# Performance work log

Hardware: AMD Instinct MI355X
Metric: run time of the kernel (lower is better)

Reference implementation:

```python
import jax, jax.numpy as jnp
import numpy as np

EUCLIDEAN_DIM = 6
B = 1024


def _build_tables(n):
    # CGA: basis vectors e1..en, e+, e-, diagonal metric (+1)*(n+1), (-1)
    d = n + 2
    nb = 1 << d
    metric = [1] * (n + 1) + [-1]
    # clifford orders blades by (grade, lexicographic) == (popcount, bitmask)
    masks = sorted(range(nb), key=lambda m: (bin(m).count('1'), m))
    pos = {m: i for i, m in enumerate(masks)}

    def sign_of(a, b):
        # canonical reordering sign + metric contractions for common vectors
        s = 1
        aa = a >> 1
        cnt = 0
        while aa:
            cnt += bin(aa & b).count('1')
            aa >>= 1
        if cnt & 1:
            s = -s
        common = a & b
        i = 0
        while common:
            if (common & 1) and metric[i] < 0:
                s = -s
            common >>= 1
            i += 1
        return s

    nnz = nb * nb  # every basis-blade product is one signed blade (nondegenerate metric)
    left = np.empty(nnz, np.int32)
    right = np.empty(nnz, np.int32)
    res = np.empty(nnz, np.int32)
    sgn = np.empty(nnz, np.int32)
    t = 0
    for i in range(nb):
        ma = masks[i]
        for j in range(nb):
            mb = masks[j]
            left[t] = i
            right[t] = j
            res[t] = pos[ma ^ mb]
            sgn[t] = sign_of(ma, mb)
            t += 1
    grades = np.array([bin(m).count('1') for m in masks])
    point_mask = np.where(grades == 1)[0].astype(np.int32)           # grade-1 blades
    pseudo = pos[nb - 1]
    motor_mask = np.where((grades % 2 == 0) & (np.arange(nb) != pseudo))[0].astype(np.int32)
    rev = ((-1) ** ((grades * (grades - 1)) // 2)).astype(np.int32)  # reverse signs
    motor_rev = rev[motor_mask]
    return left, right, res, sgn, point_mask, motor_mask, motor_rev


def setup_inputs() -> dict:
    key = jax.random.key(0)
    k1, k2 = jax.random.split(key)
    left, right, res, sgn, pmask, mmask, mrev = _build_tables(EUCLIDEAN_DIM)
    motor = jax.random.normal(k1, (B, mmask.shape[0]), jnp.float32)
    x = jax.random.normal(k2, (B, EUCLIDEAN_DIM), jnp.float32)
    return {
        'motor': motor,
        'x': x,
        'left_idx': jnp.asarray(left),
        'right_idx': jnp.asarray(right),
        'result_idx': jnp.asarray(res),
        'signs': jnp.asarray(sgn),
        'point_mask': jnp.asarray(pmask),
        'motor_mask': jnp.asarray(mmask),
        'motor_reverse_signs': jnp.asarray(mrev),
    }


def _gp(a, b, left_idx, right_idx, result_idx, signs_f, nb):
    # gather-multiply-scatter geometric product (same pattern as torch scatter_add)
    prod = signs_f * a[:, left_idx] * b[:, right_idx]  # (B, nnz)
    return jnp.zeros((a.shape[0], nb), a.dtype).at[:, result_idx].add(prod)


def reference(motor, x, left_idx, right_idx, result_idx, signs, point_mask, motor_mask, motor_reverse_signs):
    n = EUCLIDEAN_DIM
    nb = 1 << (n + 2)
    signs_f = signs.astype(jnp.float32)
    # UPGC encode: X = [x, -0.5 + 0.5|x|^2, 0.5 + 0.5|x|^2]
    h = 0.5 * jnp.sum(x * x, axis=-1, keepdims=True)
    point = jnp.concatenate([x, h - 0.5, h + 0.5], axis=-1)  # (B, n+2)
    Bsz = motor.shape[0]
    motor_full = jnp.zeros((Bsz, nb), jnp.float32).at[:, motor_mask].set(motor)
    point_full = jnp.zeros((Bsz, nb), jnp.float32).at[:, point_mask].set(point)
    motor_rev = motor * motor_reverse_signs.astype(jnp.float32)
    motor_rev_full = jnp.zeros((Bsz, nb), jnp.float32).at[:, motor_mask].set(motor_rev)
    # sandwich product M X M~ via two sparse geometric products
    mx = _gp(motor_full, point_full, left_idx, right_idx, result_idx, signs_f, nb)
    out_full = _gp(mx, motor_rev_full, left_idx, right_idx, result_idx, signs_f, nb)
    transformed = out_full[:, point_mask]  # (B, n+2)
    # UPGC decode: first n components
    return transformed[:, :n]
```

## Files before the change

### kernel.cpp

```cpp
#include <hip/hip_runtime.h>

#define NB   256
#define NM   127
#define NP   8
#define ND   6


constexpr int popc8(int x) { int c = 0; while (x) { c += x & 1; x >>= 1; } return c; }

constexpr int sign_of(int a, int b) {
    int s = 1;
    int aa = a >> 1, cnt = 0;
    while (aa) { cnt += popc8(aa & b); aa >>= 1; }
    if (cnt & 1) s = -s;
    int common = a & b, i = 0;
    while (common) {
        if ((common & 1) && i == 7) s = -s;
        common >>= 1; ++i;
    }
    return s;
}

struct Tables {
    alignas(16) int firstT[NB * 8];
    alignas(16) int secondT[128 * 8];
    alignas(16) int mpacked[128];
    alignas(16) int invm[NB];
};

constexpr Tables build_tables() {
    Tables T{};
    int masks[NB] = {}, pos[NB] = {};
    int t = 0;
    for (int pc = 0; pc <= 8; ++pc)
        for (int m = 0; m < NB; ++m)
            if (popc8(m) == pc) masks[t++] = m;
    for (int i = 0; i < NB; ++i) pos[masks[i]] = i;

    for (int i = 0; i < NB; ++i)
        for (int k = 0; k < NP; ++k) {
            int pp = 1 + k;
            int m  = pos[masks[i] ^ masks[pp]];
            int s  = sign_of(masks[m], masks[pp]);
            T.firstT[i * 8 + k] = (m << 1) | (s < 0 ? 1 : 0);
        }

    for (int i = 0; i < NB; ++i) T.invm[i] = -1;
    int j = 0;
    for (int i = 0; i < NB; ++i) {
        int g = popc8(masks[i]);
        if ((g % 2 == 0) && masks[i] != 255) {
            int rev = ((g * (g - 1) / 2) % 2) ? -1 : 1;
            T.mpacked[j] = (i << 1) | (rev < 0 ? 1 : 0);
            T.invm[i] = j;
            for (int r = 0; r < ND; ++r) {
                int rp = 1 + r;
                int ii = pos[masks[rp] ^ masks[i]];
                int s  = sign_of(masks[ii], masks[i]);
                T.secondT[j * 8 + r] = (ii << 1) | (s < 0 ? 1 : 0);
            }
            T.secondT[j * 8 + 6] = 0;
            T.secondT[j * 8 + 7] = 0;
            ++j;
        }
    }
    return T;
}

constexpr Tables hT = build_tables();
__device__ const Tables dT = hT;

__global__ __launch_bounds__(256) void cga_apply(
    const float* __restrict__ motor,
    const float* __restrict__ x,
    float*       __restrict__ out)
{
    __shared__ float m_full[NB];
    __shared__ float mx[NB];
    __shared__ float xs[ND];
    __shared__ float wpart[4][ND];

    const int t = threadIdx.x;
    const int b = blockIdx.x;

    const int4* ft = (const int4*)dT.firstT;
    int4 f0 = ft[2 * t];
    int4 f1 = ft[2 * t + 1];

    float mv = 0.0f;
    int   mp = 0;
    int4  s0 = {0,0,0,0}, s1 = {0,0,0,0};
    if (t < NM) {
        mv = motor[b * NM + t];
        mp = dT.mpacked[t];
        const int4* st = (const int4*)dT.secondT;
        s0 = st[2 * t];
        s1 = st[2 * t + 1];
    }
    if (t < ND) xs[t] = x[b * ND + t];

    const int im = dT.invm[t];
    m_full[t] = (im >= 0) ? motor[b * NM + im] : 0.0f;
    __syncthreads();

    float pv[NP];
    float h = 0.0f;
    #pragma unroll
    for (int k = 0; k < ND; ++k) { float v = xs[k]; pv[k] = v; h += v * v; }
    h *= 0.5f;
    pv[6] = h - 0.5f;
    pv[7] = h + 0.5f;

    int fe[8] = { f0.x, f0.y, f0.z, f0.w, f1.x, f1.y, f1.z, f1.w };
    float acc = 0.0f;
    #pragma unroll
    for (int k = 0; k < NP; ++k) {
        int   m = fe[k] >> 1;
        float v = m_full[m] * pv[k];
        acc += (fe[k] & 1) ? -v : v;
    }
    mx[t] = acc;
    __syncthreads();

    float o[ND] = {0,0,0,0,0,0};
    if (t < NM) {
        float mr = (mp & 1) ? -mv : mv;
        int se[ND] = { s0.x, s0.y, s0.z, s0.w, s1.x, s1.y };
        #pragma unroll
        for (int r = 0; r < ND; ++r) {
            int   i = se[r] >> 1;
            float v = mx[i] * mr;
            o[r] += (se[r] & 1) ? -v : v;
        }
    }

    #pragma unroll
    for (int r = 0; r < ND; ++r) {
        float v = o[r];
        #pragma unroll
        for (int d = 32; d >= 1; d >>= 1) v += __shfl_down(v, d, 64);
        o[r] = v;
    }
    const int lane = t & 63, w = t >> 6;
    if (lane == 0) {
        #pragma unroll
        for (int r = 0; r < ND; ++r) wpart[w][r] = o[r];
    }
    __syncthreads();

    if (t < ND)
        out[b * ND + t] = wpart[0][t] + wpart[1][t] + wpart[2][t] + wpart[3][t];
}

extern "C" void kernel_launch(void* const* d_in, const int* in_sizes, int n_in,
                              void* d_out, int out_size, void* d_ws, size_t ws_size,
                              hipStream_t stream) {
    const float* motor = (const float*)d_in[0];
    const float* x     = (const float*)d_in[1];
    float* out = (float*)d_out;

    const int Bsz = in_sizes[0] / NM;
    cga_apply<<<Bsz, 256, 0, stream>>>(motor, x, out);
}
```

Measured before the change: 72.11 us.

## Map one batch row per wavefront and compute only odd-grade intermediate blades

Each 64-lane wavefront now handles one batch row, so a block covers four rows and the grid shrinks by a factor of four. The first product computes only the 128 odd-grade blades, indexing the compact motor array directly, which removes the scatter into a 256-entry buffer. The second product is re-partitioned so each lane accumulates 16 motor terms for one output component, with reverse signs baked into the tables and a 3-step xor shuffle reduction instead of six full reductions. This cuts wasted lanes, block-level syncs and cross-wave reductions, but it assumes the batch size is divisible by four.

```diff
diff --git a/kernel.cpp b/kernel.cpp
--- a/kernel.cpp
+++ b/kernel.cpp
@@ -1,9 +1,9 @@
 #include <hip/hip_runtime.h>
 
-#define NB   256
-#define NM   127
-#define NP   8
-#define ND   6
+#define NB  256
+#define NM  127
+#define NP  8
+#define ND  6
 
 
 constexpr int popc8(int x) { int c = 0; while (x) { c += x & 1; x >>= 1; } return c; }
@@ -22,10 +22,8 @@
 }
 
 struct Tables {
-    alignas(16) int firstT[NB * 8];
-    alignas(16) int secondT[128 * 8];
-    alignas(16) int mpacked[128];
-    alignas(16) int invm[NB];
+    alignas(16) int firstT[128 * 8];
+    alignas(16) int secondT[64 * 16];
 };
 
 constexpr Tables build_tables() {
@@ -37,31 +35,44 @@
             if (popc8(m) == pc) masks[t++] = m;
     for (int i = 0; i < NB; ++i) pos[masks[i]] = i;
 
+    int oi_of[NB] = {}; int odd_pos[128] = {}; int no = 0;
+    for (int i = 0; i < NB; ++i) oi_of[i] = -1;
     for (int i = 0; i < NB; ++i)
-        for (int k = 0; k < NP; ++k) {
-            int pp = 1 + k;
-            int m  = pos[masks[i] ^ masks[pp]];
-            int s  = sign_of(masks[m], masks[pp]);
-            T.firstT[i * 8 + k] = (m << 1) | (s < 0 ? 1 : 0);
-        }
+        if (popc8(masks[i]) & 1) { odd_pos[no] = i; oi_of[i] = no; ++no; }
 
-    for (int i = 0; i < NB; ++i) T.invm[i] = -1;
+    int invm[NB] = {}; int mpos[NM] = {}; int rev[NM] = {};
+    for (int i = 0; i < NB; ++i) invm[i] = -1;
     int j = 0;
     for (int i = 0; i < NB; ++i) {
         int g = popc8(masks[i]);
         if ((g % 2 == 0) && masks[i] != 255) {
-            int rev = ((g * (g - 1) / 2) % 2) ? -1 : 1;
-            T.mpacked[j] = (i << 1) | (rev < 0 ? 1 : 0);
-            T.invm[i] = j;
-            for (int r = 0; r < ND; ++r) {
-                int rp = 1 + r;
-                int ii = pos[masks[rp] ^ masks[i]];
-                int s  = sign_of(masks[ii], masks[i]);
-                T.secondT[j * 8 + r] = (ii << 1) | (s < 0 ? 1 : 0);
-            }
-            T.secondT[j * 8 + 6] = 0;
-            T.secondT[j * 8 + 7] = 0;
+            invm[i] = j; mpos[j] = i;
+            rev[j] = ((g * (g - 1) / 2) % 2) ? -1 : 1;
             ++j;
+        }
+    }
+
+    for (int o = 0; o < 128; ++o) {
+        int i = odd_pos[o];
+        for (int k = 0; k < NP; ++k) {
+            int pp = 1 + k;
+            int m  = pos[masks[i] ^ masks[pp]];
+            int slot = (invm[m] >= 0) ? invm[m] : 127;
+            int s  = sign_of(masks[m], masks[pp]);
+            T.firstT[o * 8 + k] = (slot << 1) | (s < 0 ? 1 : 0);
+        }
+    }
+
+    for (int l = 0; l < 64; ++l) {
+        int r = l & 7, jb = l >> 3;
+        int rr = (r < 6) ? r : 0;
+        for (int m = 0; m < 16; ++m) {
+            int jj = jb + 8 * m;
+            if (jj >= NM) { T.secondT[l * 16 + m] = 0; continue; }
+            int pj = mpos[jj];
+            int ii = pos[masks[1 + rr] ^ masks[pj]];
+            int s  = sign_of(masks[ii], masks[pj]) * rev[jj];
+            T.secondT[l * 16 + m] = (oi_of[ii] << 1) | (s < 0 ? 1 : 0);
         }
     }
     return T;
@@ -75,81 +86,69 @@
     const float* __restrict__ x,
     float*       __restrict__ out)
 {
-    __shared__ float m_full[NB];
-    __shared__ float mx[NB];
-    __shared__ float xs[ND];
-    __shared__ float wpart[4][ND];
+    __shared__ float m_s[4][128];
+    __shared__ float mxs[4][128];
 
     const int t = threadIdx.x;
-    const int b = blockIdx.x;
+    const int w = t >> 6;
+    const int l = t & 63;
+    const int row = __builtin_amdgcn_readfirstlane((int)(blockIdx.x * 4 + w));
 
-    const int4* ft = (const int4*)dT.firstT;
-    int4 f0 = ft[2 * t];
-    int4 f1 = ft[2 * t + 1];
+    const float* mrow = motor + row * NM;
+    m_s[w][l]      = mrow[l];
+    m_s[w][l + 64] = (l < 63) ? mrow[l + 64] : 0.0f;
 
-    float mv = 0.0f;
-    int   mp = 0;
-    int4  s0 = {0,0,0,0}, s1 = {0,0,0,0};
-    if (t < NM) {
-        mv = motor[b * NM + t];
-        mp = dT.mpacked[t];
-        const int4* st = (const int4*)dT.secondT;
-        s0 = st[2 * t];
-        s1 = st[2 * t + 1];
-    }
-    if (t < ND) xs[t] = x[b * ND + t];
-
-    const int im = dT.invm[t];
-    m_full[t] = (im >= 0) ? motor[b * NM + im] : 0.0f;
-    __syncthreads();
-
+    const float* xr = x + row * ND;
     float pv[NP];
     float h = 0.0f;
     #pragma unroll
-    for (int k = 0; k < ND; ++k) { float v = xs[k]; pv[k] = v; h += v * v; }
+    for (int k = 0; k < ND; ++k) { float v = xr[k]; pv[k] = v; h += v * v; }
     h *= 0.5f;
     pv[6] = h - 0.5f;
     pv[7] = h + 0.5f;
 
-    int fe[8] = { f0.x, f0.y, f0.z, f0.w, f1.x, f1.y, f1.z, f1.w };
-    float acc = 0.0f;
+    const int4* ft = (const int4*)dT.firstT;
+    int4 a0 = ft[2 * l],        a1 = ft[2 * l + 1];
+    int4 b0 = ft[2 * (l + 64)], b1 = ft[2 * (l + 64) + 1];
+    const int4* st = (const int4*)dT.secondT;
+    int4 c0 = st[4 * l], c1 = st[4 * l + 1], c2 = st[4 * l + 2], c3 = st[4 * l + 3];
+
+    __syncthreads();
+
+    int fa[8] = {a0.x, a0.y, a0.z, a0.w, a1.x, a1.y, a1.z, a1.w};
+    int fb[8] = {b0.x, b0.y, b0.z, b0.w, b1.x, b1.y, b1.z, b1.w};
+    float acc0 = 0.0f, acc1 = 0.0f;
     #pragma unroll
     for (int k = 0; k < NP; ++k) {
-        int   m = fe[k] >> 1;
-        float v = m_full[m] * pv[k];
-        acc += (fe[k] & 1) ? -v : v;
+        float v = m_s[w][fa[k] >> 1] * pv[k];
+        acc0 += (fa[k] & 1) ? -v : v;
     }
-    mx[t] = acc;
+    #pragma unroll
+    for (int k = 0; k < NP; ++k) {
+        float v = m_s[w][fb[k] >> 1] * pv[k];
+        acc1 += (fb[k] & 1) ? -v : v;
+    }
+    mxs[w][l]      = acc0;
+    mxs[w][l + 64] = acc1;
+
     __syncthreads();
 
-    float o[ND] = {0,0,0,0,0,0};
-    if (t < NM) {
-        float mr = (mp & 1) ? -mv : mv;
-        int se[ND] = { s0.x, s0.y, s0.z, s0.w, s1.x, s1.y };
-        #pragma unroll
-        for (int r = 0; r < ND; ++r) {
-            int   i = se[r] >> 1;
-            float v = mx[i] * mr;
-            o[r] += (se[r] & 1) ? -v : v;
-        }
+    const int jb = l >> 3;
+    int se[16] = {c0.x, c0.y, c0.z, c0.w, c1.x, c1.y, c1.z, c1.w,
+                  c2.x, c2.y, c2.z, c2.w, c3.x, c3.y, c3.z, c3.w};
+    float o = 0.0f;
+    #pragma unroll
+    for (int m = 0; m < 16; ++m) {
+        int e = se[m];
+        float v = mxs[w][e >> 1] * m_s[w][jb + 8 * m];
+        o += (e & 1) ? -v : v;
     }
 
-    #pragma unroll
-    for (int r = 0; r < ND; ++r) {
-        float v = o[r];
-        #pragma unroll
-        for (int d = 32; d >= 1; d >>= 1) v += __shfl_down(v, d, 64);
-        o[r] = v;
-    }
-    const int lane = t & 63, w = t >> 6;
-    if (lane == 0) {
-        #pragma unroll
-        for (int r = 0; r < ND; ++r) wpart[w][r] = o[r];
-    }
-    __syncthreads();
+    o += __shfl_xor(o, 8, 64);
+    o += __shfl_xor(o, 16, 64);
+    o += __shfl_xor(o, 32, 64);
 
-    if (t < ND)
-        out[b * ND + t] = wpart[0][t] + wpart[1][t] + wpart[2][t] + wpart[3][t];
+    if (l < ND) out[row * ND + l] = o;
 }
 
 extern "C" void kernel_launch(void* const* d_in, const int* in_sizes, int n_in,
@@ -160,5 +159,5 @@
     float* out = (float*)d_out;
 
     const int Bsz = in_sizes[0] / NM;
-    cga_apply<<<Bsz, 256, 0, stream>>>(motor, x, out);
+    cga_apply<<<Bsz / 4, 256, 0, stream>>>(motor, x, out);
 }
```

New measurement: 70.37 us. -2.4%, faster.
